# Kernel tuning notes

Measured on AMD Instinct MI355X. Metric: run time of the kernel, lower is better.

The kernel has to match this reference:

```python
import jax, jax.numpy as jnp
import numpy as np

FEAT_STRIDE = 16
SCALES = np.array([8.0, 16.0, 32.0])
RATIOS = np.array([0.5, 1.0, 2.0])
PRE_NMS_TOP_N = 6000
POST_NMS_TOP_N = 300
NMS_THRESH = 0.7


def _whctrs(anchor):
    w = anchor[2] - anchor[0] + 1.0
    h = anchor[3] - anchor[1] + 1.0
    cx = anchor[0] + 0.5 * (w - 1.0)
    cy = anchor[1] + 0.5 * (h - 1.0)
    return w, h, cx, cy


def _mkanchors(ws, hs, cx, cy):
    return np.stack([cx - 0.5 * (ws - 1.0), cy - 0.5 * (hs - 1.0),
                     cx + 0.5 * (ws - 1.0), cy + 0.5 * (hs - 1.0)], axis=1)


def generate_anchors(base_size=16, ratios=RATIOS, scales=SCALES):
    base = np.array([0.0, 0.0, base_size - 1.0, base_size - 1.0])
    w, h, cx, cy = _whctrs(base)
    size = w * h
    ws = np.round(np.sqrt(size / ratios))
    hs = np.round(ws * ratios)
    ratio_anchors = _mkanchors(ws, hs, cx, cy)
    out = []
    for a in ratio_anchors:
        w, h, cx, cy = _whctrs(a)
        out.append(_mkanchors(w * scales, h * scales, cx, cy))
    return np.vstack(out)  # (A=9, 4)


def setup_inputs():
    key = jax.random.key(0)
    k1, k2 = jax.random.split(key)
    B, A, H, W = 8, 9, 152, 152
    scores_in = jax.random.normal(k1, (B, 2 * A, H, W), jnp.float32)
    bbox_deltas = 0.5 * jax.random.normal(k2, (B, 4 * A, H, W), jnp.float32)
    im_info = jnp.tile(jnp.array([[H * FEAT_STRIDE, W * FEAT_STRIDE, 1.0]], jnp.float32), (B, 1))
    anchors = jnp.asarray(generate_anchors(), jnp.float32)
    return {"scores_in": scores_in, "bbox_deltas": bbox_deltas, "im_info": im_info, "anchors": anchors}


def bbox_transform_inv(boxes, deltas):
    w = boxes[..., 2] - boxes[..., 0] + 1.0
    h = boxes[..., 3] - boxes[..., 1] + 1.0
    cx = boxes[..., 0] + 0.5 * w
    cy = boxes[..., 1] + 0.5 * h
    dx, dy, dw, dh = deltas[..., 0], deltas[..., 1], deltas[..., 2], deltas[..., 3]
    pcx = dx * w + cx
    pcy = dy * h + cy
    pw = jnp.exp(dw) * w
    ph = jnp.exp(dh) * h
    return jnp.stack([pcx - 0.5 * pw, pcy - 0.5 * ph, pcx + 0.5 * pw, pcy + 0.5 * ph], axis=-1)


def clip_boxes(boxes, im_info):
    wmax = im_info[:, None, 1] - 1.0  # x bound, per image
    hmax = im_info[:, None, 0] - 1.0  # y bound
    x1 = jnp.minimum(jnp.maximum(boxes[..., 0], 0.0), wmax)
    y1 = jnp.minimum(jnp.maximum(boxes[..., 1], 0.0), hmax)
    x2 = jnp.minimum(jnp.maximum(boxes[..., 2], 0.0), wmax)
    y2 = jnp.minimum(jnp.maximum(boxes[..., 3], 0.0), hmax)
    return jnp.stack([x1, y1, x2, y2], axis=-1)


def nms_indices(boxes, thresh, max_out):
    # boxes: (N, 4), sorted by score descending. Greedy NMS -> up to max_out indices, -1 padded.
    x1, y1, x2, y2 = boxes[:, 0], boxes[:, 1], boxes[:, 2], boxes[:, 3]
    areas = (x2 - x1 + 1.0) * (y2 - y1 + 1.0)
    N = boxes.shape[0]

    def body(i, carry):
        suppressed, keep = carry
        idx = jnp.argmax(~suppressed)  # first surviving box = highest remaining score
        valid = ~suppressed[idx]
        keep = keep.at[i].set(jnp.where(valid, idx.astype(jnp.int32), -1))
        xx1 = jnp.maximum(x1[idx], x1)
        yy1 = jnp.maximum(y1[idx], y1)
        xx2 = jnp.minimum(x2[idx], x2)
        yy2 = jnp.minimum(y2[idx], y2)
        inter = jnp.maximum(xx2 - xx1 + 1.0, 0.0) * jnp.maximum(yy2 - yy1 + 1.0, 0.0)
        iou = inter / (areas[idx] + areas - inter)
        suppressed = jnp.where(valid, suppressed | (iou > thresh), suppressed)
        return suppressed, keep

    _, keep = jax.lax.fori_loop(0, max_out, body,
                                (jnp.zeros(N, bool), jnp.full(max_out, -1, jnp.int32)))
    return keep


def _forward(scores_in, bbox_deltas, im_info, anchors):
    B, _, H, W = scores_in.shape
    A = anchors.shape[0]
    # fg objectness scores: channels [A:2A] -> (B, K*A) in (row, col, anchor) order
    scores = scores_in[:, A:].transpose(0, 2, 3, 1).reshape(B, -1)
    deltas = bbox_deltas.transpose(0, 2, 3, 1).reshape(B, -1, 4)
    sx = (jnp.arange(W) * FEAT_STRIDE).astype(jnp.float32)
    sy = (jnp.arange(H) * FEAT_STRIDE).astype(jnp.float32)
    gx, gy = jnp.meshgrid(sx, sy)  # (H, W)
    shifts = jnp.stack([gx.ravel(), gy.ravel(), gx.ravel(), gy.ravel()], axis=1)  # (K, 4)
    all_anchors = (anchors[None, :, :] + shifts[:, None, :]).reshape(-1, 4)  # (K*A, 4)
    proposals = bbox_transform_inv(all_anchors[None], deltas)  # (B, K*A, 4)
    proposals = clip_boxes(proposals, im_info)
    _, order = jax.lax.top_k(scores, PRE_NMS_TOP_N)  # descending, == sorted order truncated
    props_top = jnp.take_along_axis(proposals, order[..., None], axis=1)  # (B, PRE, 4)
    keep = jax.vmap(lambda b: nms_indices(b, NMS_THRESH, POST_NMS_TOP_N))(props_top)  # (B, POST)
    valid = keep >= 0
    sel = jnp.take_along_axis(props_top, jnp.maximum(keep, 0)[..., None], axis=1)
    sel = jnp.where(valid[..., None], sel, 0.0)
    batch_col = jnp.broadcast_to(jnp.arange(B, dtype=jnp.float32)[:, None, None],
                                 (B, POST_NMS_TOP_N, 1))
    return jnp.concatenate([batch_col, sel], axis=2)  # (B, POST, 5)


def reference(scores_in, bbox_deltas, im_info, anchors):
    return _forward(scores_in, bbox_deltas, im_info, anchors)
```

## Files before the change

### kernel.cpp

```cpp
#include <hip/hip_runtime.h>
#include <stdint.h>

#define H_ 152
#define W_ 152
#define A_ 9
#define HW_ (H_ * W_)
#define N_ (HW_ * A_)
#define B_ 8
#define PRE_TOP 6000
#define POST_TOP 300
#define NBUCK 4096
#define NFINE 32768
#define CAND_CAP 8192
#define NMS_TH 0.7f
#define CNT_STRIDE 32
#define RTILE 512

#define OFF_HIST    0
#define OFF_SSUF    131072
#define OFF_CNT     262144
#define OFF_CAND    263168
#define OFF_GROUP   787456
#define OFF_BOXES   1311744
#define OFF_CANDBOX 2079744
#define WS_NEED     (2079744ull + 1048576ull)


__device__ __forceinline__ unsigned fkey(float f) {
    unsigned u = __float_as_uint(f);
    return (u & 0x80000000u) ? ~u : (u | 0x80000000u);
}

__device__ __forceinline__ bool sup_test(float ax1, float ay1, float ax2, float ay2, float aar,
                                         float bx1, float by1, float bx2, float by2, float bar) {
    float xx1 = fmaxf(ax1, bx1);
    float yy1 = fmaxf(ay1, by1);
    float xx2 = fminf(ax2, bx2);
    float yy2 = fminf(ay2, by2);
    float iw = fmaxf(xx2 - xx1 + 1.0f, 0.0f);
    float ih = fmaxf(yy2 - yy1 + 1.0f, 0.0f);
    float inter = __fmul_rn(iw, ih);
    float iou = inter / (aar + bar - inter);
    return iou > NMS_TH;
}

__device__ __forceinline__ float4 decode_box(float an0, float an1, float an2, float an3,
                                             float sx, float sy,
                                             float dx, float dy, float dw, float dh,
                                             float wmax, float hmax) {
    float ax1 = an0 + sx;
    float ay1 = an1 + sy;
    float ax2 = an2 + sx;
    float ay2 = an3 + sy;
    float ww = ax2 - ax1 + 1.0f;
    float hh = ay2 - ay1 + 1.0f;
    float ctx = ax1 + 0.5f * ww;
    float cty = ay1 + 0.5f * hh;
    float pcx = __fadd_rn(__fmul_rn(dx, ww), ctx);
    float pcy = __fadd_rn(__fmul_rn(dy, hh), cty);
    float pw = __fmul_rn(expf(dw), ww);
    float ph = __fmul_rn(expf(dh), hh);
    float x1 = pcx - 0.5f * pw;
    float y1 = pcy - 0.5f * ph;
    float x2 = pcx + 0.5f * pw;
    float y2 = pcy + 0.5f * ph;
    x1 = fminf(fmaxf(x1, 0.0f), wmax);
    y1 = fminf(fmaxf(y1, 0.0f), hmax);
    x2 = fminf(fmaxf(x2, 0.0f), wmax);
    y2 = fminf(fmaxf(y2, 0.0f), hmax);
    return make_float4(x1, y1, x2, y2);
}


__global__ void zero2_k(unsigned* __restrict__ base, unsigned* __restrict__ p2) {
    const int n1 = 263168 / 4;
    const int n2 = 768000 / 4;
    int i = blockIdx.x * blockDim.x + threadIdx.x;
    int st = gridDim.x * blockDim.x;
    for (int k = i; k < n1 + n2; k += st) {
        if (k < n1) base[k] = 0u;
        else p2[k - n1] = 0u;
    }
}

__global__ void hist_k(const float* __restrict__ scores, unsigned* __restrict__ hist) {
    __shared__ unsigned lh[NBUCK];
    int b = blockIdx.y;
    for (int i = threadIdx.x; i < NBUCK; i += blockDim.x) lh[i] = 0;
    __syncthreads();
    const float4* sb = (const float4*)(scores + ((size_t)b * 18 + A_) * HW_);
    const int N4 = N_ / 4;
    int stride = gridDim.x * blockDim.x;
    for (int e = blockIdx.x * blockDim.x + threadIdx.x; e < N4; e += stride) {
        float4 v = sb[e];
        atomicAdd(&lh[fkey(v.x) >> 20], 1u);
        atomicAdd(&lh[fkey(v.y) >> 20], 1u);
        atomicAdd(&lh[fkey(v.z) >> 20], 1u);
        atomicAdd(&lh[fkey(v.w) >> 20], 1u);
    }
    __syncthreads();
    for (int i = threadIdx.x; i < NBUCK; i += blockDim.x) {
        unsigned v = lh[i];
        if (v) atomicAdd(&hist[b * NBUCK + i], v);
    }
}

__global__ void scan_k(const unsigned* __restrict__ hist, unsigned* __restrict__ bucketT) {
    __shared__ unsigned ps[1024];
    int b = blockIdx.x, t = threadIdx.x;
    const unsigned* hb = hist + b * NBUCK;
    unsigned c0 = hb[4095 - (4 * t + 0)];
    unsigned c1 = hb[4095 - (4 * t + 1)];
    unsigned c2 = hb[4095 - (4 * t + 2)];
    unsigned c3 = hb[4095 - (4 * t + 3)];
    unsigned local = c0 + c1 + c2 + c3;
    ps[t] = local;
    __syncthreads();
    for (int off = 1; off < 1024; off <<= 1) {
        unsigned v = (t >= off) ? ps[t - off] : 0u;
        __syncthreads();
        ps[t] += v;
        __syncthreads();
    }
    unsigned incl = ps[t], excl = incl - local;
    if (excl < PRE_TOP && incl >= PRE_TOP) {
        unsigned cum = excl;
        unsigned cc[4] = {c0, c1, c2, c3};
#pragma unroll
        for (int k = 0; k < 4; ++k) {
            cum += cc[k];
            if (cum >= PRE_TOP) { bucketT[b] = (unsigned)(4095 - (4 * t + k)); break; }
        }
    }
    if (t == 1023 && ps[1023] < PRE_TOP) bucketT[b] = 0;
}

__global__ void compact_k(const float* __restrict__ scores, const float* __restrict__ deltas,
                          const float* __restrict__ anchors, const float* __restrict__ im_info,
                          const unsigned* __restrict__ bucketT,
                          unsigned* __restrict__ cnt, uint2* __restrict__ cand,
                          float4* __restrict__ candbox) {
    __shared__ unsigned wtot[4], wbase[4];
    __shared__ unsigned blkbase;
    int b = blockIdx.y;
    const float4* sb = (const float4*)(scores + ((size_t)b * 18 + A_) * HW_);
    const float* db = deltas + (size_t)b * 36 * HW_;
    float hmax = im_info[b * 3 + 0] - 1.0f;
    float wmax = im_info[b * 3 + 1] - 1.0f;
    unsigned T = bucketT[b];
    int lane = threadIdx.x & 63;
    int wid = threadIdx.x >> 6;
    const int N4 = N_ / 4;
    int stride = gridDim.x * blockDim.x;
    int niters = (N4 + stride - 1) / stride;
    unsigned long long lower = (lane == 63) ? 0x7fffffffffffffffull
                                            : ((1ull << lane) - 1ull);
    uint2* cb = cand + (size_t)b * CAND_CAP;
    float4* cx = candbox + (size_t)b * CAND_CAP;
    for (int it = 0; it < niters; ++it) {
        int e = it * stride + blockIdx.x * (int)blockDim.x + (int)threadIdx.x;
        bool p0 = false, p1 = false, p2 = false, p3 = false;
        unsigned k0 = 0, k1 = 0, k2 = 0, k3 = 0;
        if (e < N4) {
            float4 v = sb[e];
            k0 = fkey(v.x); k1 = fkey(v.y); k2 = fkey(v.z); k3 = fkey(v.w);
            p0 = (k0 >> 20) >= T; p1 = (k1 >> 20) >= T;
            p2 = (k2 >> 20) >= T; p3 = (k3 >> 20) >= T;
        }
        unsigned long long m0 = __ballot(p0), m1 = __ballot(p1);
        unsigned long long m2 = __ballot(p2), m3 = __ballot(p3);
        unsigned t0 = (unsigned)__popcll(m0), t1 = (unsigned)__popcll(m1);
        unsigned t2 = (unsigned)__popcll(m2), t3 = (unsigned)__popcll(m3);
        unsigned wtotal = t0 + t1 + t2 + t3;
        if (lane == 0) wtot[wid] = wtotal;
        __syncthreads();
        if (threadIdx.x == 0) {
            unsigned s0 = wtot[0], s1 = wtot[1], s2 = wtot[2], s3 = wtot[3];
            unsigned tot = s0 + s1 + s2 + s3;
            blkbase = tot ? atomicAdd(&cnt[b * CNT_STRIDE], tot) : 0u;
            wbase[0] = 0; wbase[1] = s0; wbase[2] = s0 + s1; wbase[3] = s0 + s1 + s2;
        }
        __syncthreads();
        if (wtotal) {
            unsigned base = blkbase + wbase[wid];
            unsigned o0 = base + (unsigned)__popcll(m0 & lower);
            unsigned o1 = base + t0 + (unsigned)__popcll(m1 & lower);
            unsigned o2 = base + t0 + t1 + (unsigned)__popcll(m2 & lower);
            unsigned o3 = base + t0 + t1 + t2 + (unsigned)__popcll(m3 & lower);
            int e4 = e * 4;
#define EMIT(P, O, K, IDX)                                                      \
            if (P && O < CAND_CAP) {                                            \
                int a = (IDX) / HW_, pix = (IDX) - a * HW_;                     \
                cb[O] = make_uint2(K, (unsigned)(pix * A_ + a));                \
                int didx = (4 * a) * HW_ + pix;                                 \
                float dx = db[didx];                                            \
                float dy = db[didx + HW_];                                      \
                float dw = db[didx + 2 * HW_];                                  \
                float dh = db[didx + 3 * HW_];                                  \
                int w = pix % W_, h = pix / W_;                                 \
                cx[O] = decode_box(anchors[a * 4 + 0], anchors[a * 4 + 1],      \
                                   anchors[a * 4 + 2], anchors[a * 4 + 3],      \
                                   (float)(w * 16), (float)(h * 16),            \
                                   dx, dy, dw, dh, wmax, hmax);                 \
            }
            EMIT(p0, o0, k0, e4 + 0)
            EMIT(p1, o1, k1, e4 + 1)
            EMIT(p2, o2, k2, e4 + 2)
            EMIT(p3, o3, k3, e4 + 3)
#undef EMIT
        }
    }
}

__global__ void __launch_bounds__(1024) finesort_k(const unsigned* __restrict__ cnt,
                                                   uint2* __restrict__ cand,
                                                   unsigned long long* __restrict__ grouped,
                                                   ushort* __restrict__ slot16all) {
    __shared__ unsigned lh[NFINE];
    __shared__ unsigned ps[1024];
    int b = blockIdx.x, t = threadIdx.x;
    int M = min((int)cnt[b * CNT_STRIDE], CAND_CAP);
    uint2* cb = cand + (size_t)b * CAND_CAP;
    unsigned long long* g = grouped + (size_t)b * CAND_CAP;
    ushort* slot16 = slot16all + (size_t)b * CAND_CAP;
    for (int i = t; i < NFINE; i += 1024) lh[i] = 0u;
    __syncthreads();
    for (int i = t; i < M; i += 1024) {
        unsigned key16 = cb[i].x >> 16;
        unsigned f = (key16 >= 32768u) ? (key16 - 32768u) : 0u;
        atomicAdd(&lh[f], 1u);
    }
    __syncthreads();
    unsigned c[32];
    unsigned local = 0;
#pragma unroll
    for (int k = 0; k < 32; ++k) { c[k] = lh[32767 - (32 * t + k)]; local += c[k]; }
    ps[t] = local;
    __syncthreads();
    for (int off = 1; off < 1024; off <<= 1) {
        unsigned v = (t >= off) ? ps[t - off] : 0u;
        __syncthreads();
        ps[t] += v;
        __syncthreads();
    }
    unsigned run = ps[t] - local;
    __syncthreads();
#pragma unroll
    for (int k = 0; k < 32; ++k) {
        lh[32767 - (32 * t + k)] = run;
        run += c[k];
    }
    __syncthreads();
    for (int i = t; i < M; i += 1024) {
        uint2 cd = cb[i];
        unsigned key16 = cd.x >> 16;
        unsigned f = (key16 >= 32768u) ? (key16 - 32768u) : 0u;
        unsigned pos = atomicAdd(&lh[f], 1u);
        if (pos < CAND_CAP) {
            g[pos] = ((unsigned long long)cd.x << 32) | (unsigned)(~cd.y);
            slot16[pos] = (ushort)i;
        }
    }
    __syncthreads();
    ushort* S16 = (ushort*)cb;
    for (int i = t; i < NFINE; i += 1024)
        S16[i] = (ushort)min(lh[i], 65535u);
}

__global__ void __launch_bounds__(256) rank_k(const unsigned* __restrict__ cnt,
                                              const unsigned long long* __restrict__ grouped,
                                              const ushort* __restrict__ S16all,
                                              const ushort* __restrict__ slot16all,
                                              const float4* __restrict__ candbox,
                                              float4* __restrict__ boxes) {
    __shared__ unsigned long long tile[RTILE];
    __shared__ int s_rs, s_re;
    int b = blockIdx.y, t = threadIdx.x;
    int M = min((int)cnt[b * CNT_STRIDE], CAND_CAP);
    int c0 = blockIdx.x * 256;
    if (c0 >= M) return;
    const unsigned long long* g = grouped + (size_t)b * CAND_CAP;
    const ushort* S16 = S16all + (size_t)b * NFINE;
    const ushort* slot16 = slot16all + (size_t)b * CAND_CAP;
    const float4* cx = candbox + (size_t)b * CAND_CAP;
    int i = c0 + t;
    bool valid = i < M;
    unsigned long long comp = valid ? g[i] : 0ull;

    float4 pre = make_float4(0.f, 0.f, 0.f, 0.f);
    if (valid) pre = cx[slot16[i]];

    unsigned key16 = (unsigned)(comp >> 48);
    int f = (key16 >= 32768u) ? (int)(key16 - 32768u) : 0;
    int bs = 0, be = 0;
    if (valid) {
        bs = (f < 32767) ? min((int)S16[f + 1], M) : 0;
        be = min((int)S16[f], M);
    }
    if (t == 0) {
        unsigned kf = (unsigned)(g[c0] >> 48);
        int bf = (kf >= 32768u) ? (int)(kf - 32768u) : 0;
        int last = min(c0 + 255, M - 1);
        unsigned kl = (unsigned)(g[last] >> 48);
        int bl = (kl >= 32768u) ? (int)(kl - 32768u) : 0;
        s_rs = (bf < 32767) ? min((int)S16[bf + 1], M) : 0;
        s_re = min((int)S16[bl], M);
    }
    __syncthreads();
    int rs = s_rs, re = s_re;
    int cgt = 0;
    for (int tb = rs; tb < re; tb += RTILE) {
        int navail = min(RTILE, re - tb);
        __syncthreads();
        for (int j = t; j < navail; j += 256) tile[j] = g[tb + j];
        __syncthreads();
        if (valid) {
            int lo = max(bs, tb) - tb;
            int hi = min(be, tb + navail) - tb;
            int a0 = 0, a1 = 0, a2 = 0, a3 = 0, a4 = 0, a5 = 0, a6 = 0, a7 = 0;
            int j = lo;
            for (; j + 8 <= hi; j += 8) {
                unsigned long long v0 = tile[j + 0];
                unsigned long long v1 = tile[j + 1];
                unsigned long long v2 = tile[j + 2];
                unsigned long long v3 = tile[j + 3];
                unsigned long long v4 = tile[j + 4];
                unsigned long long v5 = tile[j + 5];
                unsigned long long v6 = tile[j + 6];
                unsigned long long v7 = tile[j + 7];
                a0 += (v0 > comp); a1 += (v1 > comp); a2 += (v2 > comp); a3 += (v3 > comp);
                a4 += (v4 > comp); a5 += (v5 > comp); a6 += (v6 > comp); a7 += (v7 > comp);
            }
            for (; j < hi; ++j) cgt += (tile[j] > comp);
            cgt += (a0 + a1 + a2 + a3) + (a4 + a5 + a6 + a7);
        }
    }
    if (!valid) return;
    int rank = bs + cgt;
    if (rank >= PRE_TOP) return;
    boxes[(size_t)b * PRE_TOP + rank] = pre;
}

__global__ void __launch_bounds__(1024) nms_k(const float4* __restrict__ boxes,
                                              float* __restrict__ out) {
    __shared__ float4 kbox[POST_TOP];
    __shared__ float  karea[POST_TOP];
    __shared__ float4 gbox4[64];
    __shared__ float  gar[64];
    __shared__ unsigned extw[2];
    __shared__ unsigned intraw[128];
    __shared__ unsigned long long s_keep;
    __shared__ int s_base, s_kc, s_done;
    int b = blockIdx.x, t = threadIdx.x;
    int lane = t & 63, w = t >> 6;
    if (t == 0) { s_kc = 0; s_done = 0; }
    const float4* bb = boxes + (size_t)b * PRE_TOP;
    const int ngroups = (PRE_TOP + 63) / 64;

    float4 vcur = make_float4(0.f, 0.f, 0.f, 0.f);
    if (t < 64) vcur = bb[t];

    for (int g = 0; g < ngroups; ++g) {
        __syncthreads();
        if (s_done) break;
        int gbase = g * 64;
        int gsz = min(64, PRE_TOP - gbase);
        if (t < gsz) {
            gbox4[t] = vcur;
            gar[t] = __fmul_rn(vcur.z - vcur.x + 1.0f, vcur.w - vcur.y + 1.0f);
        }
        if (t < 64) {
            int nidx = min(gbase + 64 + t, PRE_TOP - 1);
            vcur = bb[nidx];
        }
        if (t < 2) extw[t] = 0u;
        if (t < 128) intraw[t] = 0u;
        __syncthreads();

        int kc = s_kc;
        {
            int j = t >> 4, sub = t & 15;
            if (j < gsz) {
                float4 cb4 = gbox4[j];
                float car = gar[j];
                bool any = false;
                for (int kk = sub; kk < kc && !any; kk += 16) {
                    float4 kb = kbox[kk];
                    float ka = karea[kk];
                    any = sup_test(kb.x, kb.y, kb.z, kb.w, ka,
                                   cb4.x, cb4.y, cb4.z, cb4.w, car);
                }
                if (any) atomicOr(&extw[j >> 5], 1u << (j & 31));
            }
        }
        {
            float4 mb = gbox4[lane];
            float mar = gar[lane];
#pragma unroll
            for (int it = 0; it < 4; ++it) {
                int jj = w + it * 16;
                float4 bj = gbox4[jj];
                float baj = gar[jj];
                bool sup = (jj < lane) && (lane < gsz) && (jj < gsz) &&
                           sup_test(bj.x, bj.y, bj.z, bj.w, baj,
                                    mb.x, mb.y, mb.z, mb.w, mar);
                unsigned long long m = __ballot(sup);
                if (lane == 0 && (unsigned)m) atomicOr(&intraw[2 * jj], (unsigned)m);
                if (lane == 1 && (unsigned)(m >> 32))
                    atomicOr(&intraw[2 * jj + 1], (unsigned)(m >> 32));
            }
        }
        __syncthreads();

        if (t == 0) {
            unsigned long long ext64 = (unsigned long long)extw[0] |
                                       ((unsigned long long)extw[1] << 32);
            unsigned long long validm = (gsz >= 64) ? ~0ull : ((1ull << gsz) - 1ull);
            unsigned long long alive = (~ext64) & validm;
            unsigned long long keep = 0ull;
            int kcc = s_kc;
            s_base = kcc;
            while (alive && kcc < POST_TOP) {
                int j = __ffsll((long long)alive) - 1;
                keep |= (1ull << j);
                ++kcc;
                unsigned long long row = (unsigned long long)intraw[2 * j] |
                                         ((unsigned long long)intraw[2 * j + 1] << 32);
                alive &= ~row;
                alive &= ~(1ull << j);
            }
            s_keep = keep;
            s_kc = kcc;
            if (kcc >= POST_TOP) s_done = 1;
        }
        __syncthreads();

        if (t < gsz && ((s_keep >> t) & 1ull)) {
            int rank = __popcll(s_keep & ((1ull << t) - 1ull));
            int slot = s_base + rank;
            float4 mb = gbox4[t];
            kbox[slot] = mb;
            karea[slot] = gar[t];
            float* o = out + (size_t)(b * POST_TOP + slot) * 5;
            o[0] = (float)b; o[1] = mb.x; o[2] = mb.y; o[3] = mb.z; o[4] = mb.w;
        }
    }
    __syncthreads();
    for (int sl = s_kc + t; sl < POST_TOP; sl += 1024) {
        float* o = out + (size_t)(b * POST_TOP + sl) * 5;
        o[0] = (float)b; o[1] = 0.f; o[2] = 0.f; o[3] = 0.f; o[4] = 0.f;
    }
}


extern "C" void kernel_launch(void* const* d_in, const int* in_sizes, int n_in,
                              void* d_out, int out_size, void* d_ws, size_t ws_size,
                              hipStream_t stream) {
    const float* scores  = (const float*)d_in[0];
    const float* deltas  = (const float*)d_in[1];
    const float* im_info = (const float*)d_in[2];
    const float* anchors = (const float*)d_in[3];
    float* out = (float*)d_out;

    unsigned*           hist    = (unsigned*)((char*)d_ws + OFF_HIST);
    unsigned*           cnt     = (unsigned*)((char*)d_ws + OFF_CNT);
    uint2*              cand    = (uint2*)((char*)d_ws + OFF_CAND);
    unsigned long long* grouped = (unsigned long long*)((char*)d_ws + OFF_GROUP);
    float4*             boxes   = (float4*)((char*)d_ws + OFF_BOXES);
    float4*             candbox = (float4*)((char*)d_ws + OFF_CANDBOX);
    ushort*             slot16  = (ushort*)((char*)d_ws + OFF_HIST);
    unsigned*           bucketT = cnt + B_ * CNT_STRIDE - 8;

    zero2_k<<<128, 256, 0, stream>>>((unsigned*)d_ws, (unsigned*)((char*)d_ws + OFF_BOXES));
    hist_k<<<dim3(64, B_), 256, 0, stream>>>(scores, hist);
    scan_k<<<B_, 1024, 0, stream>>>(hist, bucketT);
    compact_k<<<dim3(64, B_), 256, 0, stream>>>(scores, deltas, anchors, im_info,
                                                bucketT, cnt, cand, candbox);
    finesort_k<<<B_, 1024, 0, stream>>>(cnt, cand, grouped, slot16);
    rank_k<<<dim3(32, B_), 256, 0, stream>>>(cnt, grouped, (const ushort*)cand,
                                             slot16, candbox, boxes);
    nms_k<<<B_, 1024, 0, stream>>>(boxes, out);
}
```

Before: 98.31 us.

## Fuse histogram with threshold scan and fine sort with rank into single kernels

```diff
diff --git a/kernel.cpp b/kernel.cpp
--- a/kernel.cpp
+++ b/kernel.cpp
@@ -14,15 +14,12 @@
 #define CAND_CAP 8192
 #define NMS_TH 0.7f
 #define CNT_STRIDE 32
-#define RTILE 512
 
 #define OFF_HIST    0
-#define OFF_SSUF    131072
 #define OFF_CNT     262144
-#define OFF_CAND    263168
-#define OFF_GROUP   787456
 #define OFF_BOXES   1311744
 #define OFF_CANDBOX 2079744
+#define OFF_CAND    263168
 #define WS_NEED     (2079744ull + 1048576ull)
 
 
@@ -72,26 +69,28 @@
 }
 
 
-__global__ void zero2_k(unsigned* __restrict__ base, unsigned* __restrict__ p2) {
-    const int n1 = 263168 / 4;
-    const int n2 = 768000 / 4;
+__global__ void zero_k(unsigned* __restrict__ ws) {
+    unsigned* cntr = (unsigned*)((char*)ws + OFF_CNT);
     int i = blockIdx.x * blockDim.x + threadIdx.x;
     int st = gridDim.x * blockDim.x;
-    for (int k = i; k < n1 + n2; k += st) {
-        if (k < n1) base[k] = 0u;
-        else p2[k - n1] = 0u;
-    }
-}
-
-__global__ void hist_k(const float* __restrict__ scores, unsigned* __restrict__ hist) {
+    for (int k = i; k < 32768 + 256; k += st) {
+        if (k < 32768) ws[k] = 0u;
+        else cntr[k - 32768] = 0u;
+    }
+}
+
+__global__ void hist_scan_k(const float* __restrict__ scores, unsigned* __restrict__ hist,
+                            unsigned* __restrict__ done, unsigned* __restrict__ bucketT) {
     __shared__ unsigned lh[NBUCK];
-    int b = blockIdx.y;
-    for (int i = threadIdx.x; i < NBUCK; i += blockDim.x) lh[i] = 0;
+    __shared__ unsigned ps[256];
+    __shared__ int s_last;
+    int b = blockIdx.y, t = threadIdx.x;
+    for (int i = t; i < NBUCK; i += blockDim.x) lh[i] = 0;
     __syncthreads();
     const float4* sb = (const float4*)(scores + ((size_t)b * 18 + A_) * HW_);
     const int N4 = N_ / 4;
     int stride = gridDim.x * blockDim.x;
-    for (int e = blockIdx.x * blockDim.x + threadIdx.x; e < N4; e += stride) {
+    for (int e = blockIdx.x * blockDim.x + t; e < N4; e += stride) {
         float4 v = sb[e];
         atomicAdd(&lh[fkey(v.x) >> 20], 1u);
         atomicAdd(&lh[fkey(v.y) >> 20], 1u);
@@ -99,24 +98,28 @@
         atomicAdd(&lh[fkey(v.w) >> 20], 1u);
     }
     __syncthreads();
-    for (int i = threadIdx.x; i < NBUCK; i += blockDim.x) {
+    unsigned* hb = hist + b * NBUCK;
+    for (int i = t; i < NBUCK; i += blockDim.x) {
         unsigned v = lh[i];
-        if (v) atomicAdd(&hist[b * NBUCK + i], v);
-    }
-}
-
-__global__ void scan_k(const unsigned* __restrict__ hist, unsigned* __restrict__ bucketT) {
-    __shared__ unsigned ps[1024];
-    int b = blockIdx.x, t = threadIdx.x;
-    const unsigned* hb = hist + b * NBUCK;
-    unsigned c0 = hb[4095 - (4 * t + 0)];
-    unsigned c1 = hb[4095 - (4 * t + 1)];
-    unsigned c2 = hb[4095 - (4 * t + 2)];
-    unsigned c3 = hb[4095 - (4 * t + 3)];
-    unsigned local = c0 + c1 + c2 + c3;
+        if (v) atomicAdd(&hb[i], v);
+    }
+    __syncthreads();
+    __threadfence();
+    if (t == 0) s_last = (atomicAdd(&done[b], 1u) == (unsigned)(gridDim.x - 1));
+    __syncthreads();
+    if (!s_last) return;
+
+    unsigned c[16];
+    unsigned local = 0;
+#pragma unroll
+    for (int k = 0; k < 16; ++k) {
+        int f = 4095 - (16 * t + k);
+        c[k] = __hip_atomic_load(&hb[f], __ATOMIC_RELAXED, __HIP_MEMORY_SCOPE_AGENT);
+        local += c[k];
+    }
     ps[t] = local;
     __syncthreads();
-    for (int off = 1; off < 1024; off <<= 1) {
+    for (int off = 1; off < 256; off <<= 1) {
         unsigned v = (t >= off) ? ps[t - off] : 0u;
         __syncthreads();
         ps[t] += v;
@@ -125,14 +128,13 @@
     unsigned incl = ps[t], excl = incl - local;
     if (excl < PRE_TOP && incl >= PRE_TOP) {
         unsigned cum = excl;
-        unsigned cc[4] = {c0, c1, c2, c3};
 #pragma unroll
-        for (int k = 0; k < 4; ++k) {
-            cum += cc[k];
-            if (cum >= PRE_TOP) { bucketT[b] = (unsigned)(4095 - (4 * t + k)); break; }
-        }
-    }
-    if (t == 1023 && ps[1023] < PRE_TOP) bucketT[b] = 0;
+        for (int k = 0; k < 16; ++k) {
+            cum += c[k];
+            if (cum >= PRE_TOP) { bucketT[b] = (unsigned)(4095 - (16 * t + k)); break; }
+        }
+    }
+    if (t == 255 && ps[255] < PRE_TOP) bucketT[b] = 0;
 }
 
 __global__ void compact_k(const float* __restrict__ scores, const float* __restrict__ deltas,
@@ -212,29 +214,32 @@
     }
 }
 
-__global__ void __launch_bounds__(1024) finesort_k(const unsigned* __restrict__ cnt,
-                                                   uint2* __restrict__ cand,
-                                                   unsigned long long* __restrict__ grouped,
-                                                   ushort* __restrict__ slot16all) {
-    __shared__ unsigned lh[NFINE];
+__global__ void __launch_bounds__(1024) sortrank_k(const unsigned* __restrict__ cnt,
+                                                   const uint2* __restrict__ cand,
+                                                   const float4* __restrict__ candbox,
+                                                   float4* __restrict__ boxes) {
+    __shared__ unsigned lh32[NFINE / 2];
+    __shared__ unsigned long long gl[CAND_CAP];
     __shared__ unsigned ps[1024];
     int b = blockIdx.x, t = threadIdx.x;
     int M = min((int)cnt[b * CNT_STRIDE], CAND_CAP);
-    uint2* cb = cand + (size_t)b * CAND_CAP;
-    unsigned long long* g = grouped + (size_t)b * CAND_CAP;
-    ushort* slot16 = slot16all + (size_t)b * CAND_CAP;
-    for (int i = t; i < NFINE; i += 1024) lh[i] = 0u;
+    const uint2* cb = cand + (size_t)b * CAND_CAP;
+    for (int i = t; i < NFINE / 2; i += 1024) lh32[i] = 0u;
     __syncthreads();
     for (int i = t; i < M; i += 1024) {
         unsigned key16 = cb[i].x >> 16;
         unsigned f = (key16 >= 32768u) ? (key16 - 32768u) : 0u;
-        atomicAdd(&lh[f], 1u);
+        atomicAdd(&lh32[f & 16383u], 1u << (16u * (f >> 14)));
     }
     __syncthreads();
     unsigned c[32];
     unsigned local = 0;
 #pragma unroll
-    for (int k = 0; k < 32; ++k) { c[k] = lh[32767 - (32 * t + k)]; local += c[k]; }
+    for (int k = 0; k < 32; ++k) {
+        unsigned f = 32767u - (32u * t + k);
+        c[k] = (lh32[f & 16383u] >> (16u * (f >> 14))) & 0xFFFFu;
+        local += c[k];
+    }
     ps[t] = local;
     __syncthreads();
     for (int off = 1; off < 1024; off <<= 1) {
@@ -245,9 +250,12 @@
     }
     unsigned run = ps[t] - local;
     __syncthreads();
+    for (int i = t; i < NFINE / 2; i += 1024) lh32[i] = 0u;
+    __syncthreads();
 #pragma unroll
     for (int k = 0; k < 32; ++k) {
-        lh[32767 - (32 * t + k)] = run;
+        unsigned f = 32767u - (32u * t + k);
+        if (run) atomicOr(&lh32[f & 16383u], (run & 0xFFFFu) << (16u * (f >> 14)));
         run += c[k];
     }
     __syncthreads();
@@ -255,90 +263,45 @@
         uint2 cd = cb[i];
         unsigned key16 = cd.x >> 16;
         unsigned f = (key16 >= 32768u) ? (key16 - 32768u) : 0u;
-        unsigned pos = atomicAdd(&lh[f], 1u);
-        if (pos < CAND_CAP) {
-            g[pos] = ((unsigned long long)cd.x << 32) | (unsigned)(~cd.y);
-            slot16[pos] = (ushort)i;
-        }
-    }
-    __syncthreads();
-    ushort* S16 = (ushort*)cb;
-    for (int i = t; i < NFINE; i += 1024)
-        S16[i] = (ushort)min(lh[i], 65535u);
-}
-
-__global__ void __launch_bounds__(256) rank_k(const unsigned* __restrict__ cnt,
-                                              const unsigned long long* __restrict__ grouped,
-                                              const ushort* __restrict__ S16all,
-                                              const ushort* __restrict__ slot16all,
-                                              const float4* __restrict__ candbox,
-                                              float4* __restrict__ boxes) {
-    __shared__ unsigned long long tile[RTILE];
-    __shared__ int s_rs, s_re;
-    int b = blockIdx.y, t = threadIdx.x;
-    int M = min((int)cnt[b * CNT_STRIDE], CAND_CAP);
-    int c0 = blockIdx.x * 256;
-    if (c0 >= M) return;
-    const unsigned long long* g = grouped + (size_t)b * CAND_CAP;
-    const ushort* S16 = S16all + (size_t)b * NFINE;
-    const ushort* slot16 = slot16all + (size_t)b * CAND_CAP;
+        unsigned sh = 16u * (f >> 14);
+        unsigned old = atomicAdd(&lh32[f & 16383u], 1u << sh);
+        unsigned pos = (old >> sh) & 0xFFFFu;
+        if (pos < CAND_CAP)
+            gl[pos] = ((unsigned long long)cd.x << 32) |
+                      ((unsigned long long)((~cd.y) & 0x3FFFFu) << 14) |
+                      (unsigned long long)i;
+    }
+    __syncthreads();
     const float4* cx = candbox + (size_t)b * CAND_CAP;
-    int i = c0 + t;
-    bool valid = i < M;
-    unsigned long long comp = valid ? g[i] : 0ull;
-
-    float4 pre = make_float4(0.f, 0.f, 0.f, 0.f);
-    if (valid) pre = cx[slot16[i]];
-
-    unsigned key16 = (unsigned)(comp >> 48);
-    int f = (key16 >= 32768u) ? (int)(key16 - 32768u) : 0;
-    int bs = 0, be = 0;
-    if (valid) {
-        bs = (f < 32767) ? min((int)S16[f + 1], M) : 0;
-        be = min((int)S16[f], M);
-    }
-    if (t == 0) {
-        unsigned kf = (unsigned)(g[c0] >> 48);
-        int bf = (kf >= 32768u) ? (int)(kf - 32768u) : 0;
-        int last = min(c0 + 255, M - 1);
-        unsigned kl = (unsigned)(g[last] >> 48);
-        int bl = (kl >= 32768u) ? (int)(kl - 32768u) : 0;
-        s_rs = (bf < 32767) ? min((int)S16[bf + 1], M) : 0;
-        s_re = min((int)S16[bl], M);
-    }
-    __syncthreads();
-    int rs = s_rs, re = s_re;
-    int cgt = 0;
-    for (int tb = rs; tb < re; tb += RTILE) {
-        int navail = min(RTILE, re - tb);
-        __syncthreads();
-        for (int j = t; j < navail; j += 256) tile[j] = g[tb + j];
-        __syncthreads();
-        if (valid) {
-            int lo = max(bs, tb) - tb;
-            int hi = min(be, tb + navail) - tb;
-            int a0 = 0, a1 = 0, a2 = 0, a3 = 0, a4 = 0, a5 = 0, a6 = 0, a7 = 0;
-            int j = lo;
-            for (; j + 8 <= hi; j += 8) {
-                unsigned long long v0 = tile[j + 0];
-                unsigned long long v1 = tile[j + 1];
-                unsigned long long v2 = tile[j + 2];
-                unsigned long long v3 = tile[j + 3];
-                unsigned long long v4 = tile[j + 4];
-                unsigned long long v5 = tile[j + 5];
-                unsigned long long v6 = tile[j + 6];
-                unsigned long long v7 = tile[j + 7];
-                a0 += (v0 > comp); a1 += (v1 > comp); a2 += (v2 > comp); a3 += (v3 > comp);
-                a4 += (v4 > comp); a5 += (v5 > comp); a6 += (v6 > comp); a7 += (v7 > comp);
-            }
-            for (; j < hi; ++j) cgt += (tile[j] > comp);
-            cgt += (a0 + a1 + a2 + a3) + (a4 + a5 + a6 + a7);
-        }
-    }
-    if (!valid) return;
-    int rank = bs + cgt;
-    if (rank >= PRE_TOP) return;
-    boxes[(size_t)b * PRE_TOP + rank] = pre;
+    for (int i = t; i < M; i += 1024) {
+        unsigned long long comp = gl[i];
+        unsigned key16 = (unsigned)(comp >> 48);
+        int f = (key16 >= 32768u) ? (int)(key16 - 32768u) : 0;
+        unsigned shf = 16u * ((unsigned)f >> 14);
+        int be = (int)((lh32[(unsigned)f & 16383u] >> shf) & 0xFFFFu);
+        int bs = 0;
+        if (f < 32767) {
+            int f1 = f + 1;
+            unsigned sh1 = 16u * ((unsigned)f1 >> 14);
+            bs = (int)((lh32[(unsigned)f1 & 16383u] >> sh1) & 0xFFFFu);
+        }
+        be = min(be, M); bs = min(bs, M);
+        int cgt = 0, j = bs;
+        int a0 = 0, a1 = 0, a2 = 0, a3 = 0;
+        for (; j + 4 <= be; j += 4) {
+            a0 += (gl[j + 0] > comp);
+            a1 += (gl[j + 1] > comp);
+            a2 += (gl[j + 2] > comp);
+            a3 += (gl[j + 3] > comp);
+        }
+        for (; j < be; ++j) cgt += (gl[j] > comp);
+        cgt += a0 + a1 + a2 + a3;
+        int rank = bs + cgt;
+        if (rank < PRE_TOP) {
+            unsigned slot = (unsigned)(comp & 0x3FFFull);
+            boxes[(size_t)b * PRE_TOP + rank] = cx[slot];
+        }
+    }
 }
 
 __global__ void __launch_bounds__(1024) nms_k(const float4* __restrict__ boxes,
@@ -462,22 +425,18 @@
     const float* anchors = (const float*)d_in[3];
     float* out = (float*)d_out;
 
-    unsigned*           hist    = (unsigned*)((char*)d_ws + OFF_HIST);
-    unsigned*           cnt     = (unsigned*)((char*)d_ws + OFF_CNT);
-    uint2*              cand    = (uint2*)((char*)d_ws + OFF_CAND);
-    unsigned long long* grouped = (unsigned long long*)((char*)d_ws + OFF_GROUP);
-    float4*             boxes   = (float4*)((char*)d_ws + OFF_BOXES);
-    float4*             candbox = (float4*)((char*)d_ws + OFF_CANDBOX);
-    ushort*             slot16  = (ushort*)((char*)d_ws + OFF_HIST);
-    unsigned*           bucketT = cnt + B_ * CNT_STRIDE - 8;
-
-    zero2_k<<<128, 256, 0, stream>>>((unsigned*)d_ws, (unsigned*)((char*)d_ws + OFF_BOXES));
-    hist_k<<<dim3(64, B_), 256, 0, stream>>>(scores, hist);
-    scan_k<<<B_, 1024, 0, stream>>>(hist, bucketT);
+    unsigned* hist    = (unsigned*)((char*)d_ws + OFF_HIST);
+    unsigned* cnt     = (unsigned*)((char*)d_ws + OFF_CNT);
+    uint2*    cand    = (uint2*)((char*)d_ws + OFF_CAND);
+    float4*   boxes   = (float4*)((char*)d_ws + OFF_BOXES);
+    float4*   candbox = (float4*)((char*)d_ws + OFF_CANDBOX);
+    unsigned* done    = cnt + 240;
+    unsigned* bucketT = cnt + 248;
+
+    zero_k<<<32, 256, 0, stream>>>((unsigned*)d_ws);
+    hist_scan_k<<<dim3(64, B_), 256, 0, stream>>>(scores, hist, done, bucketT);
     compact_k<<<dim3(64, B_), 256, 0, stream>>>(scores, deltas, anchors, im_info,
                                                 bucketT, cnt, cand, candbox);
-    finesort_k<<<B_, 1024, 0, stream>>>(cnt, cand, grouped, slot16);
-    rank_k<<<dim3(32, B_), 256, 0, stream>>>(cnt, grouped, (const ushort*)cand,
-                                             slot16, candbox, boxes);
+    sortrank_k<<<B_, 1024, 0, stream>>>(cnt, cand, candbox, boxes);
     nms_k<<<B_, 1024, 0, stream>>>(boxes, out);
 }
```

Result: slower. 146.5 us (+49.0%).
